# Performance work log

Hardware: AMD Instinct MI355X
Metric: run time of the kernel (lower is better)

Reference implementation:

```python
import jax, jax.numpy as jnp
import numpy as np

N = 100000
E = 1600000
D_PCA = 50
D_BIO = 64
HID = 32
HEADS = 4
OUT = 50
EPS = 1e-5


def setup_inputs() -> dict:
    key = jax.random.key(0)
    ks = jax.random.split(key, 32)
    g = lambda i, shape, s=0.05: jax.random.normal(ks[i], shape, dtype=jnp.float32) * s
    inp = {
        'x_pca': jax.random.normal(ks[0], (N, D_PCA), dtype=jnp.float32),
        'x_bio': jax.random.normal(ks[1], (N, D_BIO), dtype=jnp.float32),
        'edge_index': jax.random.randint(ks[2], (2, E), 0, N, dtype=jnp.int32),
        # bio encoder: Linear(64,16) -> BN(16) -> ELU -> Linear(16,16) -> ELU
        'bioW1': g(3, (16, D_BIO)), 'biob1': g(4, (16,)),
        'bn0_g': 1.0 + g(5, (16,)), 'bn0_b': g(6, (16,)),
        'bn0_m': g(7, (16,)), 'bn0_v': 1.0 + 0.1 * jax.random.uniform(ks[8], (16,), dtype=jnp.float32),
        'bioW2': g(9, (16, 16)), 'biob2': g(10, (16,)),
        # GATv2 layer 1: in = 50+16 = 66, out = HEADS*HID concat
        'Wl1': g(11, (HEADS * HID, D_PCA + 16)), 'bl1': g(12, (HEADS * HID,)),
        'Wr1': g(13, (HEADS * HID, D_PCA + 16)), 'br1': g(14, (HEADS * HID,)),
        'att1': g(15, (HEADS, HID)), 'bias1': g(16, (HEADS * HID,)),
        'bn1_g': 1.0 + g(17, (HEADS * HID,)), 'bn1_b': g(18, (HEADS * HID,)),
        'bn1_m': g(19, (HEADS * HID,)), 'bn1_v': 1.0 + 0.1 * jax.random.uniform(ks[20], (HEADS * HID,), dtype=jnp.float32),
        # GATv2 layer 2: in = HEADS*HID, heads=1, concat=False
        'Wl2': g(21, (HID, HEADS * HID)), 'bl2': g(22, (HID,)),
        'Wr2': g(23, (HID, HEADS * HID)), 'br2': g(24, (HID,)),
        'att2': g(25, (1, HID)), 'bias2': g(26, (HID,)),
        'bn2_g': 1.0 + g(27, (HID,)), 'bn2_b': g(28, (HID,)),
        'bn2_m': g(29, (HID,)), 'bn2_v': 1.0 + 0.1 * jax.random.uniform(ks[30], (HID,), dtype=jnp.float32),
        'predW': g(31, (OUT, HID)), 'predb': jnp.zeros((OUT,), dtype=jnp.float32),
    }
    return inp


def _bn(h, gm, bt, mean, var):
    # BatchNorm1d in eval mode (running stats)
    return (h - mean) * jax.lax.rsqrt(var + EPS) * gm + bt


def _gatv2(x, src, dst, Wl, bl, Wr, br, att, bias, heads, out_dim, concat):
    n = x.shape[0]
    xl = (x @ Wl.T + bl).reshape(n, heads, out_dim)  # source transform
    xr = (x @ Wr.T + br).reshape(n, heads, out_dim)  # target transform
    e = jax.nn.leaky_relu(xl[src] + xr[dst], 0.2)    # [E,H,C]
    logits = jnp.einsum('ehc,hc->eh', e, att)        # [E,H]
    m = jax.ops.segment_max(logits, dst, num_segments=n)
    a = jnp.exp(logits - m[dst])
    denom = jax.ops.segment_sum(a, dst, num_segments=n)
    alpha = a / (denom[dst] + 1e-16)                 # segment softmax over dst
    out = jax.ops.segment_sum(xl[src] * alpha[..., None], dst, num_segments=n)
    out = out.reshape(n, heads * out_dim) if concat else out.mean(axis=1)
    return out + bias


def reference(x_pca, x_bio, edge_index,
              bioW1, biob1, bn0_g, bn0_b, bn0_m, bn0_v, bioW2, biob2,
              Wl1, bl1, Wr1, br1, att1, bias1, bn1_g, bn1_b, bn1_m, bn1_v,
              Wl2, bl2, Wr2, br2, att2, bias2, bn2_g, bn2_b, bn2_m, bn2_v,
              predW, predb):
    n = x_pca.shape[0]
    # add self-loops (PyG GATv2Conv default)
    loop = jnp.arange(n, dtype=edge_index.dtype)
    src = jnp.concatenate([edge_index[0], loop])
    dst = jnp.concatenate([edge_index[1], loop])

    # bio encoder
    h_bio = jax.nn.elu(_bn(x_bio @ bioW1.T + biob1, bn0_g, bn0_b, bn0_m, bn0_v))
    h_bio = jax.nn.elu(h_bio @ bioW2.T + biob2)
    x = jnp.concatenate([x_pca, h_bio], axis=1)  # [N, 66]

    h = _gatv2(x, src, dst, Wl1, bl1, Wr1, br1, att1, bias1, HEADS, HID, True)
    h = jax.nn.elu(_bn(h, bn1_g, bn1_b, bn1_m, bn1_v))  # dropout off (eval)
    h = _gatv2(h, src, dst, Wl2, bl2, Wr2, br2, att2, bias2, 1, HID, False)
    h = jax.nn.elu(_bn(h, bn2_g, bn2_b, bn2_m, bn2_v))
    return h @ predW.T + predb
```

## Files before the change

kernel.cpp:

```cpp
#include <hip/hip_runtime.h>
#include <hip/hip_fp16.h>
#include <cstdint>
#include <cstddef>

#define NN 100000
#define NE 1600000
#define NEP (NE + NN)
#define NBLK 200
#define CHUNK ((NEP + NBLK - 1) / NBLK)
#define NBUCK2 ((NN + 255) / 256)
#define HISTN (NBUCK2 * NBLK)
#define HSCAN_BLOCKS ((HISTN + 1023) / 1024)

typedef __attribute__((ext_vector_type(8))) _Float16 half8;
typedef __attribute__((ext_vector_type(4))) _Float16 h4v;
typedef __attribute__((ext_vector_type(2))) _Float16 h2v;
typedef __attribute__((ext_vector_type(4))) float float4v;

__device__ __forceinline__ float elu_f(float x) {
    return x > 0.f ? x : __expf(x) - 1.f;
}

template<int CTRL>
__device__ __forceinline__ float dpp_add(float x) {
    int s = __builtin_amdgcn_update_dpp(0, __float_as_int(x), CTRL, 0xF, 0xF, true);
    return x + __int_as_float(s);
}
__device__ __forceinline__ float sum8_all(float x) {
    x = dpp_add<0xB1>(x); x = dpp_add<0x4E>(x); x = dpp_add<0x141>(x);
    return x;
}
__device__ __forceinline__ float sum16_all(float x) {
    x = dpp_add<0xB1>(x); x = dpp_add<0x4E>(x); x = dpp_add<0x141>(x); x = dpp_add<0x140>(x);
    return x;
}

__device__ __forceinline__ float dot2f(h2v a, h2v b, float c) {
#if __has_builtin(__builtin_amdgcn_fdot2)
    return __builtin_amdgcn_fdot2(a, b, c, false);
#else
    return fmaf((float)a[0], (float)b[0], fmaf((float)a[1], (float)b[1], c));
#endif
}

__device__ __forceinline__ h2v hmax2v(h2v a, h2v b) {
#if __has_builtin(__builtin_elementwise_max)
    return __builtin_elementwise_max(a, b);
#else
    __half2 r = __hmax2(*(__half2*)&a, *(__half2*)&b);
    return *(h2v*)&r;
#endif
}


__global__ __launch_bounds__(256) void part_hist(const int* __restrict__ ei, int* __restrict__ hist)
{
    __shared__ int cnt[NBUCK2];
    int tid = threadIdx.x, k = blockIdx.x;
    for (int i = tid; i < NBUCK2; i += 256) cnt[i] = 0;
    __syncthreads();
    int e0 = k * CHUNK, e1 = min(e0 + CHUNK, NEP);
    for (int e = e0 + tid; e < e1; e += 256) {
        int dst = (e < NE) ? ei[NE + e] : e - NE;
        atomicAdd(&cnt[dst >> 8], 1);
    }
    __syncthreads();
    for (int i = tid; i < NBUCK2; i += 256) hist[i * NBLK + k] = cnt[i];
}

__global__ __launch_bounds__(256) void scan_p1(const int* __restrict__ src, int* __restrict__ part, int n)
{
    __shared__ int wsum[4];
    int t = threadIdx.x;
    int i0 = blockIdx.x * 1024 + t * 4;
    int s = 0;
    if (i0 + 3 < n) { int4 d = *(const int4*)(src + i0); s = d.x + d.y + d.z + d.w; }
    else { for (int k = 0; k < 4; k++) if (i0 + k < n) s += src[i0 + k]; }
    for (int d = 1; d < 64; d <<= 1) s += __shfl_xor(s, d, 64);
    if ((t & 63) == 0) wsum[t >> 6] = s;
    __syncthreads();
    if (t == 0) part[blockIdx.x] = wsum[0] + wsum[1] + wsum[2] + wsum[3];
}

__global__ __launch_bounds__(128) void scan_p2(int* __restrict__ part, int nb, int* __restrict__ off)
{
    __shared__ int wt[2];
    int t = threadIdx.x;
    int lane = t & 63, w = t >> 6;
    int v = (t < nb) ? part[t] : 0;
    int x = v;
    for (int d = 1; d < 64; d <<= 1) { int y = __shfl_up(x, d, 64); if (lane >= d) x += y; }
    if (lane == 63) wt[w] = x;
    __syncthreads();
    int base = (w == 1) ? wt[0] : 0;
    int excl = base + x - v;
    if (t < nb) part[t] = excl;
    if (t == 0) off[NN] = NEP;
}

__global__ __launch_bounds__(256) void scan_p3(int* __restrict__ data, const int* __restrict__ part, int n)
{
    __shared__ int wsum[4];
    int t = threadIdx.x, lane = t & 63, w = t >> 6;
    int i0 = blockIdx.x * 1024 + t * 4;
    int d0 = 0, d1 = 0, d2 = 0, d3 = 0;
    if (i0 + 3 < n) { int4 d = *(const int4*)(data + i0); d0 = d.x; d1 = d.y; d2 = d.z; d3 = d.w; }
    else if (i0 < n) {
        d0 = data[i0];
        if (i0 + 1 < n) d1 = data[i0 + 1];
        if (i0 + 2 < n) d2 = data[i0 + 2];
    }
    int s = d0 + d1 + d2 + d3;
    int x = s;
    for (int d = 1; d < 64; d <<= 1) { int y = __shfl_up(x, d, 64); if (lane >= d) x += y; }
    if (lane == 63) wsum[w] = x;
    __syncthreads();
    int wb = 0;
    for (int i = 0; i < w; i++) wb += wsum[i];
    int base = part[blockIdx.x] + wb + x - s;
    if (i0 < n)     data[i0]     = base;
    if (i0 + 1 < n) data[i0 + 1] = base + d0;
    if (i0 + 2 < n) data[i0 + 2] = base + d0 + d1;
    if (i0 + 3 < n) data[i0 + 3] = base + d0 + d1 + d2;
}

__global__ __launch_bounds__(256) void part_scatter(const int* __restrict__ ei,
                                                    const int* __restrict__ hist,
                                                    unsigned* __restrict__ ebuf)
{
    __shared__ int cur[NBUCK2];
    int tid = threadIdx.x, k = blockIdx.x;
    for (int i = tid; i < NBUCK2; i += 256) cur[i] = hist[i * NBLK + k];
    __syncthreads();
    int e0 = k * CHUNK, e1 = min(e0 + CHUNK, NEP);
    for (int e = e0 + tid; e < e1; e += 256) {
        int src, dst;
        if (e < NE) { src = ei[e]; dst = ei[NE + e]; } else { src = dst = e - NE; }
        int pos = atomicAdd(&cur[dst >> 8], 1);
        ebuf[pos] = (unsigned)src | ((unsigned)(dst & 255) << 24);
    }
}

__global__ __launch_bounds__(256) void bucket_csr(const int* __restrict__ hist,
                                                  const unsigned* __restrict__ ebuf,
                                                  int* __restrict__ off, int* __restrict__ csr)
{
    __shared__ int cnt[256];
    __shared__ int cur[256];
    __shared__ int wsum[4];
    int b = blockIdx.x;
    int d0 = b << 8;
    int tid = threadIdx.x;
    int e0 = hist[b * NBLK];
    int e1 = (b + 1 < NBUCK2) ? hist[(b + 1) * NBLK] : NEP;
    cnt[tid] = 0;
    __syncthreads();
    for (int i = e0 + tid; i < e1; i += 256) atomicAdd(&cnt[ebuf[i] >> 24], 1);
    __syncthreads();
    int c = cnt[tid];
    int x = c;
    int lane = tid & 63, w = tid >> 6;
    for (int d = 1; d < 64; d <<= 1) { int y = __shfl_up(x, d, 64); if (lane >= d) x += y; }
    if (lane == 63) wsum[w] = x;
    __syncthreads();
    int wb = 0;
    for (int i = 0; i < w; i++) wb += wsum[i];
    int excl = wb + x - c;
    cur[tid] = e0 + excl;
    int node = d0 + tid;
    if (node < NN) off[node] = e0 + excl;
    __syncthreads();
    for (int i = e0 + tid; i < e1; i += 256) {
        unsigned v = ebuf[i];
        int p = atomicAdd(&cur[v >> 24], 1);
        csr[p] = (int)(v & 0xFFFFFF);
    }
}


__global__ __launch_bounds__(256) void bio_kernel(
    const float* __restrict__ xb, const float* __restrict__ xp,
    const float* __restrict__ W1, const float* __restrict__ b1,
    const float* __restrict__ g0, const float* __restrict__ bb0,
    const float* __restrict__ m0, const float* __restrict__ v0,
    const float* __restrict__ W2, const float* __restrict__ b2,
    __half* __restrict__ xh)
{
    __shared__ float sW1[16*64], sW2[16*16], sb1[16], sb2[16], ss[16], st[16];
    int tid = threadIdx.x;
    for (int idx = tid; idx < 1024; idx += 256) sW1[idx] = W1[idx];
    if (tid < 256) sW2[tid] = W2[tid];
    if (tid < 16) {
        sb1[tid] = b1[tid]; sb2[tid] = b2[tid];
        float s = g0[tid] * rsqrtf(v0[tid] + 1e-5f);
        ss[tid] = s; st[tid] = bb0[tid] - m0[tid] * s;
    }
    __syncthreads();
    int i = blockIdx.x * 256 + tid;
    if (i >= NN) return;
    float bio[64];
    const float4* p = (const float4*)(xb + (size_t)i * 64);
    #pragma unroll
    for (int q = 0; q < 16; q++) {
        float4 f = p[q];
        bio[q*4] = f.x; bio[q*4+1] = f.y; bio[q*4+2] = f.z; bio[q*4+3] = f.w;
    }
    float t1[16];
    #pragma unroll
    for (int j = 0; j < 16; j++) {
        float acc = sb1[j];
        #pragma unroll
        for (int k = 0; k < 64; k++) acc += bio[k] * sW1[j*64 + k];
        acc = acc * ss[j] + st[j];
        t1[j] = elu_f(acc);
    }
    __half* xrow = xh + (size_t)i * 96;
    const float* xpr = xp + (size_t)i * 50;
    #pragma unroll
    for (int j = 0; j < 25; j++) {
        float2 f = *(const float2*)(xpr + 2 * j);
        *(__half2*)(xrow + 2 * j) = __floats2half2_rn(f.x, f.y);
    }
    #pragma unroll
    for (int j = 0; j < 16; j++) {
        float acc = sb2[j];
        #pragma unroll
        for (int k = 0; k < 16; k++) acc += t1[k] * sW2[j*16 + k];
        xrow[50 + j] = __float2half(elu_f(acc));
    }
    __half2 z2 = __floats2half2_rn(0.f, 0.f);
    #pragma unroll
    for (int j = 0; j < 15; j++) *(__half2*)(xrow + 66 + 2 * j) = z2;
}


__global__ __launch_bounds__(256) void wconvert_all(
    const float* __restrict__ Wl1, const float* __restrict__ Wr1,
    const float* __restrict__ bl1, const float* __restrict__ br1,
    const float* __restrict__ Wl2, const float* __restrict__ Wr2,
    const float* __restrict__ bl2, const float* __restrict__ br2,
    const float* __restrict__ predW, const float* __restrict__ predb,
    __half* __restrict__ wcat1, float* __restrict__ bcat1,
    __half* __restrict__ wcat2, float* __restrict__ bcat2,
    __half* __restrict__ wpred, float* __restrict__ bpred)
{
    int t = blockIdx.x * 256 + threadIdx.x;
    if (t < 256 * 96) {
        int j = t / 96, k = t - j * 96;
        float v = (k < 66) ? ((j < 128) ? Wl1[j * 66 + k] : Wr1[(j - 128) * 66 + k]) : 0.f;
        wcat1[t] = __float2half(v);
    }
    int u = t - 256 * 96;
    if (u >= 0 && u < 64 * 128) {
        int j = u >> 7, k = u & 127;
        float v = (j < 32) ? Wl2[j * 128 + k] : Wr2[(j - 32) * 128 + k];
        wcat2[u] = __float2half(v);
    }
    int w = u - 64 * 128;
    if (w >= 0 && w < 64 * 32) {
        int j = w >> 5;
        wpred[w] = __float2half(j < 50 ? predW[w] : 0.f);
    }
    int z = w - 64 * 32;
    if (z >= 0 && z < 256) bcat1[z] = (z < 128) ? bl1[z] : br1[z - 128];
    int z2 = z - 256;
    if (z2 >= 0 && z2 < 64) bcat2[z2] = (z2 < 32) ? bl2[z2] : br2[z2 - 32];
    int z3 = z2 - 64;
    if (z3 >= 0 && z3 < 64) bpred[z3] = (z3 < 50) ? predb[z3] : 0.f;
}

template<int KT, int NC, bool FOUT>
__global__ __launch_bounds__(256) void mfma_gemm(
    const __half* __restrict__ in, const __half* __restrict__ wcat,
    const float* __restrict__ bcat, void* __restrict__ outv, int n, int ncol)
{
    constexpr int K = KT * 32;
    constexpr int KP = K + 8;
    __shared__ __half sW[NC * KP];
    __shared__ __half sX[64 * KP];
    __shared__ float sB[NC];
    int tid = threadIdx.x;
    for (int idx = tid * 8; idx < NC * K; idx += 256 * 8) {
        int r = idx / K, c = idx - r * K;
        *(half8*)(&sW[r * KP + c]) = *(const half8*)(&wcat[r * K + c]);
    }
    for (int idx = tid; idx < NC; idx += 256) sB[idx] = bcat[idx];
    int row0 = blockIdx.x * 64;
    half8 hz = {0, 0, 0, 0, 0, 0, 0, 0};
    for (int idx = tid * 8; idx < 64 * K; idx += 256 * 8) {
        int r = idx / K, c = idx - r * K;
        int gr = row0 + r;
        half8 v = (gr < n) ? *(const half8*)(&in[(size_t)gr * K + c]) : hz;
        *(half8*)(&sX[r * KP + c]) = v;
    }
    __syncthreads();
    int w = tid >> 6, lane = tid & 63;
    int m = lane & 15, quad = lane >> 4;
    half8 a[KT];
    #pragma unroll
    for (int kt = 0; kt < KT; kt++)
        a[kt] = *(const half8*)(&sX[(w * 16 + m) * KP + kt * 32 + quad * 8]);
    #pragma unroll 1
    for (int nt = 0; nt < NC / 16; nt++) {
        float4v acc = {0.f, 0.f, 0.f, 0.f};
        #pragma unroll
        for (int kt = 0; kt < KT; kt++) {
            half8 bfrag = *(const half8*)(&sW[(nt * 16 + m) * KP + kt * 32 + quad * 8]);
            acc = __builtin_amdgcn_mfma_f32_16x16x32_f16(a[kt], bfrag, acc, 0, 0, 0);
        }
        int col = nt * 16 + m;
        float bias = sB[col];
        #pragma unroll
        for (int i = 0; i < 4; i++) {
            int r = row0 + w * 16 + quad * 4 + i;
            if (r < n) {
                if (FOUT) { if (col < ncol) ((float*)outv)[(size_t)r * ncol + col] = acc[i] + bias; }
                else ((__half*)outv)[(size_t)r * NC + col] = __float2half(acc[i] + bias);
            }
        }
    }
}

__global__ __launch_bounds__(256) void fused_gat1(
    const int* __restrict__ off, const int* __restrict__ csr,
    const __half* __restrict__ xcat, const float* __restrict__ att,
    const float* __restrict__ bias, const float* __restrict__ g,
    const float* __restrict__ b, const float* __restrict__ m,
    const float* __restrict__ v, __half* __restrict__ h1)
{
    int wave = threadIdx.x >> 6;
    int lane = threadIdx.x & 63;
    int node = blockIdx.x * 4 + wave;
    if (node >= NN) return;
    int slot = lane >> 5;
    int l = lane & 31;
    int ch = l * 4;

    h4v xr4 = *(const h4v*)(xcat + (size_t)node * 256 + 128 + ch);
    h2v xr01 = {xr4[0], xr4[1]}, xr23 = {xr4[2], xr4[3]};
    float4 af = *(const float4*)(att + ch);
    h2v a01 = {(_Float16)af.x, (_Float16)af.y};
    h2v a23 = {(_Float16)af.z, (_Float16)af.w};
    const h2v c2 = {(_Float16)0.2f, (_Float16)0.2f};

    int k0 = off[node], k1 = off[node + 1];
    float acc0 = 0.f, acc1 = 0.f, acc2 = 0.f, acc3 = 0.f, denom = 0.f;

    for (int base = k0; base < k1; base += 64) {
        int nb = min(64, k1 - base);
        int mysrc = (lane < nb) ? csr[base + lane] : 0;
        int p0 = __builtin_amdgcn_readlane(mysrc, 0);
        int p1 = __builtin_amdgcn_readlane(mysrc, nb > 1 ? 1 : 0);
        int ssel = slot ? p1 : p0;
        h4v cur = *(const h4v*)(xcat + (size_t)(unsigned)ssel * 256 + ch);
        for (int t = 0; t < nb; t += 2) {
            int t2 = (t + 2 < nb) ? t + 2 : nb - 1;
            int t3 = (t + 3 < nb) ? t + 3 : nb - 1;
            int n0 = __builtin_amdgcn_readlane(mysrc, t2);
            int n1 = __builtin_amdgcn_readlane(mysrc, t3);
            int nsel = slot ? n1 : n0;
            h4v nxt = *(const h4v*)(xcat + (size_t)(unsigned)nsel * 256 + ch);

            h2v xl01 = {cur[0], cur[1]}, xl23 = {cur[2], cur[3]};
            h2v s01 = xl01 + xr01, s23 = xl23 + xr23;
            h2v ls01 = hmax2v(s01, s01 * c2);
            h2v ls23 = hmax2v(s23, s23 * c2);
            float pp = dot2f(ls01, a01, dot2f(ls23, a23, 0.f));
            pp = sum8_all(pp);
            bool valid = (t + slot) < nb;
            float wgt = valid ? __expf(pp) : 0.f;
            denom += wgt;
            acc0 = fmaf((float)cur[0], wgt, acc0);
            acc1 = fmaf((float)cur[1], wgt, acc1);
            acc2 = fmaf((float)cur[2], wgt, acc2);
            acc3 = fmaf((float)cur[3], wgt, acc3);
            cur = nxt;
        }
    }
    acc0 += __shfl_xor(acc0, 32, 64);
    acc1 += __shfl_xor(acc1, 32, 64);
    acc2 += __shfl_xor(acc2, 32, 64);
    acc3 += __shfl_xor(acc3, 32, 64);
    denom += __shfl_xor(denom, 32, 64);
    if (slot == 0) {
        float inv = 1.f / (denom + 1e-16f);
        float4 gv = *(const float4*)(g + ch);
        float4 vv = *(const float4*)(v + ch);
        float4 bv = *(const float4*)(b + ch);
        float4 mv = *(const float4*)(m + ch);
        float4 biv = *(const float4*)(bias + ch);
        float s0 = gv.x * rsqrtf(vv.x + 1e-5f);
        float s1 = gv.y * rsqrtf(vv.y + 1e-5f);
        float s2 = gv.z * rsqrtf(vv.z + 1e-5f);
        float s3 = gv.w * rsqrtf(vv.w + 1e-5f);
        float o0 = elu_f((acc0 * inv + biv.x) * s0 + (bv.x - mv.x * s0));
        float o1 = elu_f((acc1 * inv + biv.y) * s1 + (bv.y - mv.y * s1));
        float o2 = elu_f((acc2 * inv + biv.z) * s2 + (bv.z - mv.z * s2));
        float o3 = elu_f((acc3 * inv + biv.w) * s3 + (bv.w - mv.w * s3));
        h4v o = {(_Float16)o0, (_Float16)o1, (_Float16)o2, (_Float16)o3};
        *(h4v*)(h1 + (size_t)node * 128 + ch) = o;
    }
}

__global__ __launch_bounds__(256) void fused_gat2(
    const int* __restrict__ off, const int* __restrict__ csr,
    const __half* __restrict__ xcat2, const float* __restrict__ att,
    const float* __restrict__ bias, const float* __restrict__ g,
    const float* __restrict__ b, const float* __restrict__ m,
    const float* __restrict__ v, __half* __restrict__ h2)
{
    int wave = threadIdx.x >> 6;
    int lane = threadIdx.x & 63;
    int node = blockIdx.x * 4 + wave;
    if (node >= NN) return;
    int row = lane >> 4;
    int cp  = lane & 15;
    int c   = cp * 2;

    h2v xr = *(const h2v*)(xcat2 + (size_t)node * 64 + 32 + c);
    float2 af = *(const float2*)(att + c);
    h2v ah = {(_Float16)af.x, (_Float16)af.y};
    const h2v c2 = {(_Float16)0.2f, (_Float16)0.2f};

    int k0 = off[node], k1 = off[node + 1];
    float accx = 0.f, accy = 0.f, denom = 0.f;

    for (int base = k0; base < k1; base += 64) {
        int nb = min(64, k1 - base);
        int mysrc = (lane < nb) ? csr[base + lane] : 0;
        for (int t = 0; t < nb; t += 4) {
            int i1 = min(t + 1, nb - 1), i2 = min(t + 2, nb - 1), i3 = min(t + 3, nb - 1);
            int s0 = __builtin_amdgcn_readlane(mysrc, t);
            int s1 = __builtin_amdgcn_readlane(mysrc, i1);
            int s2 = __builtin_amdgcn_readlane(mysrc, i2);
            int s3 = __builtin_amdgcn_readlane(mysrc, i3);
            int sa  = (row & 1) ? s1 : s0;
            int sb_ = (row & 1) ? s3 : s2;
            int ss  = (row & 2) ? sb_ : sa;
            h2v xl = *(const h2v*)(xcat2 + (size_t)(unsigned)ss * 64 + c);
            h2v s = xl + xr;
            h2v ls = hmax2v(s, s * c2);
            float pp = dot2f(ls, ah, 0.f);
            pp = sum16_all(pp);
            bool valid = (t + row) < nb;
            float wgt = valid ? __expf(pp) : 0.f;
            denom += wgt;
            accx = fmaf((float)xl[0], wgt, accx);
            accy = fmaf((float)xl[1], wgt, accy);
        }
    }
    accx  += __shfl_xor(accx, 16, 64);  accx  += __shfl_xor(accx, 32, 64);
    accy  += __shfl_xor(accy, 16, 64);  accy  += __shfl_xor(accy, 32, 64);
    denom += __shfl_xor(denom, 16, 64); denom += __shfl_xor(denom, 32, 64);
    if (row == 0) {
        float inv = 1.f / (denom + 1e-16f);
        float sC0 = g[c]     * rsqrtf(v[c]     + 1e-5f);
        float sC1 = g[c + 1] * rsqrtf(v[c + 1] + 1e-5f);
        float o0 = elu_f((accx * inv + bias[c])     * sC0 + (b[c]     - m[c]     * sC0));
        float o1 = elu_f((accy * inv + bias[c + 1]) * sC1 + (b[c + 1] - m[c + 1] * sC1));
        *(__half2*)(h2 + (size_t)node * 32 + c) = __floats2half2_rn(o0, o1);
    }
}

extern "C" void kernel_launch(void* const* d_in, const int* in_sizes, int n_in,
                              void* d_out, int out_size, void* d_ws, size_t ws_size,
                              hipStream_t stream)
{
    const float* x_pca = (const float*)d_in[0];
    const float* x_bio = (const float*)d_in[1];
    const int*   ei    = (const int*)d_in[2];
    const float* bioW1 = (const float*)d_in[3];
    const float* biob1 = (const float*)d_in[4];
    const float* bn0_g = (const float*)d_in[5];
    const float* bn0_b = (const float*)d_in[6];
    const float* bn0_m = (const float*)d_in[7];
    const float* bn0_v = (const float*)d_in[8];
    const float* bioW2 = (const float*)d_in[9];
    const float* biob2 = (const float*)d_in[10];
    const float* Wl1   = (const float*)d_in[11];
    const float* bl1   = (const float*)d_in[12];
    const float* Wr1   = (const float*)d_in[13];
    const float* br1   = (const float*)d_in[14];
    const float* att1  = (const float*)d_in[15];
    const float* bias1 = (const float*)d_in[16];
    const float* bn1_g = (const float*)d_in[17];
    const float* bn1_b = (const float*)d_in[18];
    const float* bn1_m = (const float*)d_in[19];
    const float* bn1_v = (const float*)d_in[20];
    const float* Wl2   = (const float*)d_in[21];
    const float* bl2   = (const float*)d_in[22];
    const float* Wr2   = (const float*)d_in[23];
    const float* br2   = (const float*)d_in[24];
    const float* att2  = (const float*)d_in[25];
    const float* bias2 = (const float*)d_in[26];
    const float* bn2_g = (const float*)d_in[27];
    const float* bn2_b = (const float*)d_in[28];
    const float* bn2_m = (const float*)d_in[29];
    const float* bn2_v = (const float*)d_in[30];
    const float* predW = (const float*)d_in[31];
    const float* predb = (const float*)d_in[32];

    float* ws = (float*)d_ws;
    __half* xh    = (__half*)ws;
    float*  p0    = ws + 4800000;
    __half* xcat1 = (__half*)p0;
    float*  p1    = p0 + 12800000;
    __half* h1h   = (__half*)p1;
    float*  p2    = p1 + 6400000;
    __half* xcat2 = (__half*)p2;
    float*  p3    = p2 + 3200000;
    __half* h2h   = (__half*)p3;
    float*  p4    = p3 + 1600000;
    __half* wcat1 = (__half*)p4;
    float*  bcat1 = p4 + 12288;
    __half* wcat2 = (__half*)(bcat1 + 256);
    float*  bcat2 = bcat1 + 256 + 4096;
    __half* wpred = (__half*)(bcat2 + 64);
    float*  bpred = bcat2 + 64 + 1024;
    int*    ib    = (int*)(bpred + 64);
    unsigned* ebuf = (unsigned*)ib;
    int*    hist   = ib + NEP;
    int*    part   = hist + HISTN;
    int*    off    = part + 128;
    int*    csr    = off + NN + 1;

    float* out = (float*)d_out;

    part_hist<<<NBLK, 256, 0, stream>>>(ei, hist);
    scan_p1<<<HSCAN_BLOCKS, 256, 0, stream>>>(hist, part, HISTN);
    scan_p2<<<1, 128, 0, stream>>>(part, HSCAN_BLOCKS, off);
    scan_p3<<<HSCAN_BLOCKS, 256, 0, stream>>>(hist, part, HISTN);
    part_scatter<<<NBLK, 256, 0, stream>>>(ei, hist, ebuf);
    bucket_csr<<<NBUCK2, 256, 0, stream>>>(hist, ebuf, off, csr);

    bio_kernel<<<(NN + 255) / 256, 256, 0, stream>>>(
        x_bio, x_pca, bioW1, biob1, bn0_g, bn0_b, bn0_m, bn0_v, bioW2, biob2, xh);

    wconvert_all<<<138, 256, 0, stream>>>(
        Wl1, Wr1, bl1, br1, Wl2, Wr2, bl2, br2, predW, predb,
        wcat1, bcat1, wcat2, bcat2, wpred, bpred);

    mfma_gemm<3, 256, false><<<(NN + 63) / 64, 256, 0, stream>>>(xh, wcat1, bcat1, xcat1, NN, 0);

    fused_gat1<<<(NN + 3) / 4, 256, 0, stream>>>(
        off, csr, xcat1, att1, bias1, bn1_g, bn1_b, bn1_m, bn1_v, h1h);

    mfma_gemm<4, 64, false><<<(NN + 63) / 64, 256, 0, stream>>>(h1h, wcat2, bcat2, xcat2, NN, 0);

    fused_gat2<<<(NN + 3) / 4, 256, 0, stream>>>(
        off, csr, xcat2, att2, bias2, bn2_g, bn2_b, bn2_m, bn2_v, h2h);

    mfma_gemm<1, 64, true><<<(NN + 63) / 64, 256, 0, stream>>>(h2h, wpred, bpred, out, NN, 50);
}
```

Measured before the change: 432.3 us.

## Widen per-lane gathers in GAT kernels and make GEMMs persistent with direct A loads

```diff
diff --git a/kernel.cpp b/kernel.cpp
--- a/kernel.cpp
+++ b/kernel.cpp
@@ -4,6 +4,7 @@
 #include <cstddef>
 
 #define NN 100000
+#define NROWS 100032
 #define NE 1600000
 #define NEP (NE + NN)
 #define NBLK 200
@@ -11,9 +12,9 @@
 #define NBUCK2 ((NN + 255) / 256)
 #define HISTN (NBUCK2 * NBLK)
 #define HSCAN_BLOCKS ((HISTN + 1023) / 1024)
+#define NT64 ((NN + 63) / 64)
 
 typedef __attribute__((ext_vector_type(8))) _Float16 half8;
-typedef __attribute__((ext_vector_type(4))) _Float16 h4v;
 typedef __attribute__((ext_vector_type(2))) _Float16 h2v;
 typedef __attribute__((ext_vector_type(4))) float float4v;
 
@@ -26,12 +27,9 @@
     int s = __builtin_amdgcn_update_dpp(0, __float_as_int(x), CTRL, 0xF, 0xF, true);
     return x + __int_as_float(s);
 }
-__device__ __forceinline__ float sum8_all(float x) {
-    x = dpp_add<0xB1>(x); x = dpp_add<0x4E>(x); x = dpp_add<0x141>(x);
-    return x;
-}
-__device__ __forceinline__ float sum16_all(float x) {
-    x = dpp_add<0xB1>(x); x = dpp_add<0x4E>(x); x = dpp_add<0x141>(x); x = dpp_add<0x140>(x);
+__device__ __forceinline__ float sum2_all(float x) { return dpp_add<0xB1>(x); }
+__device__ __forceinline__ float sum4_all(float x) {
+    x = dpp_add<0xB1>(x); x = dpp_add<0x4E>(x);
     return x;
 }
 
@@ -272,12 +270,11 @@
 template<int KT, int NC, bool FOUT>
 __global__ __launch_bounds__(256) void mfma_gemm(
     const __half* __restrict__ in, const __half* __restrict__ wcat,
-    const float* __restrict__ bcat, void* __restrict__ outv, int n, int ncol)
+    const float* __restrict__ bcat, void* __restrict__ outv, int n, int ncol, int ntiles)
 {
     constexpr int K = KT * 32;
     constexpr int KP = K + 8;
     __shared__ __half sW[NC * KP];
-    __shared__ __half sX[64 * KP];
     __shared__ float sB[NC];
     int tid = threadIdx.x;
     for (int idx = tid * 8; idx < NC * K; idx += 256 * 8) {
@@ -285,37 +282,32 @@
         *(half8*)(&sW[r * KP + c]) = *(const half8*)(&wcat[r * K + c]);
     }
     for (int idx = tid; idx < NC; idx += 256) sB[idx] = bcat[idx];
-    int row0 = blockIdx.x * 64;
-    half8 hz = {0, 0, 0, 0, 0, 0, 0, 0};
-    for (int idx = tid * 8; idx < 64 * K; idx += 256 * 8) {
-        int r = idx / K, c = idx - r * K;
-        int gr = row0 + r;
-        half8 v = (gr < n) ? *(const half8*)(&in[(size_t)gr * K + c]) : hz;
-        *(half8*)(&sX[r * KP + c]) = v;
-    }
     __syncthreads();
     int w = tid >> 6, lane = tid & 63;
     int m = lane & 15, quad = lane >> 4;
-    half8 a[KT];
-    #pragma unroll
-    for (int kt = 0; kt < KT; kt++)
-        a[kt] = *(const half8*)(&sX[(w * 16 + m) * KP + kt * 32 + quad * 8]);
-    #pragma unroll 1
-    for (int nt = 0; nt < NC / 16; nt++) {
-        float4v acc = {0.f, 0.f, 0.f, 0.f};
+    for (int tile = blockIdx.x; tile < ntiles; tile += gridDim.x) {
+        int arow = tile * 64 + w * 16 + m;
+        const __half* inr = in + (size_t)arow * K + quad * 8;
+        half8 a[KT];
         #pragma unroll
-        for (int kt = 0; kt < KT; kt++) {
-            half8 bfrag = *(const half8*)(&sW[(nt * 16 + m) * KP + kt * 32 + quad * 8]);
-            acc = __builtin_amdgcn_mfma_f32_16x16x32_f16(a[kt], bfrag, acc, 0, 0, 0);
-        }
-        int col = nt * 16 + m;
-        float bias = sB[col];
-        #pragma unroll
-        for (int i = 0; i < 4; i++) {
-            int r = row0 + w * 16 + quad * 4 + i;
-            if (r < n) {
-                if (FOUT) { if (col < ncol) ((float*)outv)[(size_t)r * ncol + col] = acc[i] + bias; }
-                else ((__half*)outv)[(size_t)r * NC + col] = __float2half(acc[i] + bias);
+        for (int kt = 0; kt < KT; kt++) a[kt] = *(const half8*)(inr + kt * 32);
+        #pragma unroll 1
+        for (int nt = 0; nt < NC / 16; nt++) {
+            float4v acc = {0.f, 0.f, 0.f, 0.f};
+            #pragma unroll
+            for (int kt = 0; kt < KT; kt++) {
+                half8 bfrag = *(const half8*)(&sW[(nt * 16 + m) * KP + kt * 32 + quad * 8]);
+                acc = __builtin_amdgcn_mfma_f32_16x16x32_f16(a[kt], bfrag, acc, 0, 0, 0);
+            }
+            int col = nt * 16 + m;
+            float bias = sB[col];
+            #pragma unroll
+            for (int i = 0; i < 4; i++) {
+                int r = tile * 64 + w * 16 + quad * 4 + i;
+                if (r < n) {
+                    if (FOUT) { if (col < ncol) ((float*)outv)[(size_t)r * ncol + col] = acc[i] + bias; }
+                    else ((__half*)outv)[(size_t)r * NC + col] = __float2half(acc[i] + bias);
+                }
             }
         }
     }
@@ -332,73 +324,98 @@
     int lane = threadIdx.x & 63;
     int node = blockIdx.x * 4 + wave;
     if (node >= NN) return;
-    int slot = lane >> 5;
-    int l = lane & 31;
-    int ch = l * 4;
-
-    h4v xr4 = *(const h4v*)(xcat + (size_t)node * 256 + 128 + ch);
-    h2v xr01 = {xr4[0], xr4[1]}, xr23 = {xr4[2], xr4[3]};
-    float4 af = *(const float4*)(att + ch);
-    h2v a01 = {(_Float16)af.x, (_Float16)af.y};
-    h2v a23 = {(_Float16)af.z, (_Float16)af.w};
+    int row = lane >> 3;
+    int cl  = lane & 7;
+    int ch  = cl * 16;
+
+    half8 xrA = *(const half8*)(xcat + (size_t)node * 256 + 128 + ch);
+    half8 xrB = *(const half8*)(xcat + (size_t)node * 256 + 128 + ch + 8);
+    h2v ath[8];
+    #pragma unroll
+    for (int q = 0; q < 4; q++) {
+        float4 af = *(const float4*)(att + ch + 4 * q);
+        ath[2*q]   = h2v{(_Float16)af.x, (_Float16)af.y};
+        ath[2*q+1] = h2v{(_Float16)af.z, (_Float16)af.w};
+    }
     const h2v c2 = {(_Float16)0.2f, (_Float16)0.2f};
 
     int k0 = off[node], k1 = off[node + 1];
-    float acc0 = 0.f, acc1 = 0.f, acc2 = 0.f, acc3 = 0.f, denom = 0.f;
+    float acc[16];
+    #pragma unroll
+    for (int i = 0; i < 16; i++) acc[i] = 0.f;
+    float denom = 0.f;
 
     for (int base = k0; base < k1; base += 64) {
         int nb = min(64, k1 - base);
         int mysrc = (lane < nb) ? csr[base + lane] : 0;
-        int p0 = __builtin_amdgcn_readlane(mysrc, 0);
-        int p1 = __builtin_amdgcn_readlane(mysrc, nb > 1 ? 1 : 0);
-        int ssel = slot ? p1 : p0;
-        h4v cur = *(const h4v*)(xcat + (size_t)(unsigned)ssel * 256 + ch);
-        for (int t = 0; t < nb; t += 2) {
-            int t2 = (t + 2 < nb) ? t + 2 : nb - 1;
-            int t3 = (t + 3 < nb) ? t + 3 : nb - 1;
-            int n0 = __builtin_amdgcn_readlane(mysrc, t2);
-            int n1 = __builtin_amdgcn_readlane(mysrc, t3);
-            int nsel = slot ? n1 : n0;
-            h4v nxt = *(const h4v*)(xcat + (size_t)(unsigned)nsel * 256 + ch);
-
-            h2v xl01 = {cur[0], cur[1]}, xl23 = {cur[2], cur[3]};
-            h2v s01 = xl01 + xr01, s23 = xl23 + xr23;
-            h2v ls01 = hmax2v(s01, s01 * c2);
-            h2v ls23 = hmax2v(s23, s23 * c2);
-            float pp = dot2f(ls01, a01, dot2f(ls23, a23, 0.f));
-            pp = sum8_all(pp);
-            bool valid = (t + slot) < nb;
+        int nbm1 = nb - 1;
+        int ss = __shfl(mysrc, min(row, nbm1), 64);
+        const __half* xrow0 = xcat + (size_t)(unsigned)ss * 256 + ch;
+        half8 curA = *(const half8*)xrow0;
+        half8 curB = *(const half8*)(xrow0 + 8);
+        for (int t = 0; t < nb; t += 8) {
+            int ns = __shfl(mysrc, min(t + 8 + row, nbm1), 64);
+            const __half* xrown = xcat + (size_t)(unsigned)ns * 256 + ch;
+            half8 nxtA = *(const half8*)xrown;
+            half8 nxtB = *(const half8*)(xrown + 8);
+
+            float pp = 0.f;
+            #pragma unroll
+            for (int i = 0; i < 4; i++) {
+                h2v xl = {curA[2*i], curA[2*i+1]};
+                h2v xr = {xrA[2*i], xrA[2*i+1]};
+                h2v s = xl + xr;
+                h2v l = hmax2v(s, s * c2);
+                pp = dot2f(l, ath[i], pp);
+            }
+            #pragma unroll
+            for (int i = 0; i < 4; i++) {
+                h2v xl = {curB[2*i], curB[2*i+1]};
+                h2v xr = {xrB[2*i], xrB[2*i+1]};
+                h2v s = xl + xr;
+                h2v l = hmax2v(s, s * c2);
+                pp = dot2f(l, ath[4+i], pp);
+            }
+            pp = sum2_all(pp);
+            bool valid = (t + row) < nb;
             float wgt = valid ? __expf(pp) : 0.f;
             denom += wgt;
-            acc0 = fmaf((float)cur[0], wgt, acc0);
-            acc1 = fmaf((float)cur[1], wgt, acc1);
-            acc2 = fmaf((float)cur[2], wgt, acc2);
-            acc3 = fmaf((float)cur[3], wgt, acc3);
-            cur = nxt;
+            #pragma unroll
+            for (int i = 0; i < 8; i++) acc[i] = fmaf((float)curA[i], wgt, acc[i]);
+            #pragma unroll
+            for (int i = 0; i < 8; i++) acc[8+i] = fmaf((float)curB[i], wgt, acc[8+i]);
+            curA = nxtA; curB = nxtB;
         }
     }
-    acc0 += __shfl_xor(acc0, 32, 64);
-    acc1 += __shfl_xor(acc1, 32, 64);
-    acc2 += __shfl_xor(acc2, 32, 64);
-    acc3 += __shfl_xor(acc3, 32, 64);
+    #pragma unroll
+    for (int i = 0; i < 16; i++) {
+        acc[i] += __shfl_xor(acc[i], 8, 64);
+        acc[i] += __shfl_xor(acc[i], 16, 64);
+        acc[i] += __shfl_xor(acc[i], 32, 64);
+    }
+    denom += __shfl_xor(denom, 8, 64);
+    denom += __shfl_xor(denom, 16, 64);
     denom += __shfl_xor(denom, 32, 64);
-    if (slot == 0) {
+    if (row == 0) {
         float inv = 1.f / (denom + 1e-16f);
-        float4 gv = *(const float4*)(g + ch);
-        float4 vv = *(const float4*)(v + ch);
-        float4 bv = *(const float4*)(b + ch);
-        float4 mv = *(const float4*)(m + ch);
-        float4 biv = *(const float4*)(bias + ch);
-        float s0 = gv.x * rsqrtf(vv.x + 1e-5f);
-        float s1 = gv.y * rsqrtf(vv.y + 1e-5f);
-        float s2 = gv.z * rsqrtf(vv.z + 1e-5f);
-        float s3 = gv.w * rsqrtf(vv.w + 1e-5f);
-        float o0 = elu_f((acc0 * inv + biv.x) * s0 + (bv.x - mv.x * s0));
-        float o1 = elu_f((acc1 * inv + biv.y) * s1 + (bv.y - mv.y * s1));
-        float o2 = elu_f((acc2 * inv + biv.z) * s2 + (bv.z - mv.z * s2));
-        float o3 = elu_f((acc3 * inv + biv.w) * s3 + (bv.w - mv.w * s3));
-        h4v o = {(_Float16)o0, (_Float16)o1, (_Float16)o2, (_Float16)o3};
-        *(h4v*)(h1 + (size_t)node * 128 + ch) = o;
+        _Float16 oh[16];
+        #pragma unroll
+        for (int q = 0; q < 4; q++) {
+            float4 gv = *(const float4*)(g + ch + 4*q);
+            float4 vv = *(const float4*)(v + ch + 4*q);
+            float4 bv = *(const float4*)(b + ch + 4*q);
+            float4 mv = *(const float4*)(m + ch + 4*q);
+            float4 iv = *(const float4*)(bias + ch + 4*q);
+            float sc;
+            sc = gv.x * rsqrtf(vv.x + 1e-5f); oh[4*q+0] = (_Float16)elu_f((acc[4*q+0] * inv + iv.x) * sc + (bv.x - mv.x * sc));
+            sc = gv.y * rsqrtf(vv.y + 1e-5f); oh[4*q+1] = (_Float16)elu_f((acc[4*q+1] * inv + iv.y) * sc + (bv.y - mv.y * sc));
+            sc = gv.z * rsqrtf(vv.z + 1e-5f); oh[4*q+2] = (_Float16)elu_f((acc[4*q+2] * inv + iv.z) * sc + (bv.z - mv.z * sc));
+            sc = gv.w * rsqrtf(vv.w + 1e-5f); oh[4*q+3] = (_Float16)elu_f((acc[4*q+3] * inv + iv.w) * sc + (bv.w - mv.w * sc));
+        }
+        half8 oA = {oh[0], oh[1], oh[2], oh[3], oh[4], oh[5], oh[6], oh[7]};
+        half8 oB = {oh[8], oh[9], oh[10], oh[11], oh[12], oh[13], oh[14], oh[15]};
+        *(half8*)(h1 + (size_t)node * 128 + ch) = oA;
+        *(half8*)(h1 + (size_t)node * 128 + ch + 8) = oB;
     }
 }
 
@@ -413,52 +430,83 @@
     int lane = threadIdx.x & 63;
     int node = blockIdx.x * 4 + wave;
     if (node >= NN) return;
-    int row = lane >> 4;
-    int cp  = lane & 15;
-    int c   = cp * 2;
-
-    h2v xr = *(const h2v*)(xcat2 + (size_t)node * 64 + 32 + c);
-    float2 af = *(const float2*)(att + c);
-    h2v ah = {(_Float16)af.x, (_Float16)af.y};
+    int row = lane >> 2;
+    int cl  = lane & 3;
+    int ch  = cl * 8;
+
+    half8 xr8 = *(const half8*)(xcat2 + (size_t)node * 64 + 32 + ch);
+    h2v ath[4];
+    #pragma unroll
+    for (int q = 0; q < 2; q++) {
+        float4 af = *(const float4*)(att + ch + 4 * q);
+        ath[2*q]   = h2v{(_Float16)af.x, (_Float16)af.y};
+        ath[2*q+1] = h2v{(_Float16)af.z, (_Float16)af.w};
+    }
     const h2v c2 = {(_Float16)0.2f, (_Float16)0.2f};
 
     int k0 = off[node], k1 = off[node + 1];
-    float accx = 0.f, accy = 0.f, denom = 0.f;
+    float acc[8];
+    #pragma unroll
+    for (int i = 0; i < 8; i++) acc[i] = 0.f;
+    float denom = 0.f;
 
     for (int base = k0; base < k1; base += 64) {
         int nb = min(64, k1 - base);
         int mysrc = (lane < nb) ? csr[base + lane] : 0;
-        for (int t = 0; t < nb; t += 4) {
-            int i1 = min(t + 1, nb - 1), i2 = min(t + 2, nb - 1), i3 = min(t + 3, nb - 1);
-            int s0 = __builtin_amdgcn_readlane(mysrc, t);
-            int s1 = __builtin_amdgcn_readlane(mysrc, i1);
-            int s2 = __builtin_amdgcn_readlane(mysrc, i2);
-            int s3 = __builtin_amdgcn_readlane(mysrc, i3);
-            int sa  = (row & 1) ? s1 : s0;
-            int sb_ = (row & 1) ? s3 : s2;
-            int ss  = (row & 2) ? sb_ : sa;
-            h2v xl = *(const h2v*)(xcat2 + (size_t)(unsigned)ss * 64 + c);
-            h2v s = xl + xr;
-            h2v ls = hmax2v(s, s * c2);
-            float pp = dot2f(ls, ah, 0.f);
-            pp = sum16_all(pp);
+        int nbm1 = nb - 1;
+        int ss = __shfl(mysrc, min(row, nbm1), 64);
+        half8 cur = *(const half8*)(xcat2 + (size_t)(unsigned)ss * 64 + ch);
+        for (int t = 0; t < nb; t += 16) {
+            int ns = __shfl(mysrc, min(t + 16 + row, nbm1), 64);
+            half8 nxt = *(const half8*)(xcat2 + (size_t)(unsigned)ns * 64 + ch);
+
+            float pp = 0.f;
+            #pragma unroll
+            for (int i = 0; i < 4; i++) {
+                h2v xl = {cur[2*i], cur[2*i+1]};
+                h2v xr = {xr8[2*i], xr8[2*i+1]};
+                h2v s = xl + xr;
+                h2v l = hmax2v(s, s * c2);
+                pp = dot2f(l, ath[i], pp);
+            }
+            pp = sum4_all(pp);
             bool valid = (t + row) < nb;
             float wgt = valid ? __expf(pp) : 0.f;
             denom += wgt;
-            accx = fmaf((float)xl[0], wgt, accx);
-            accy = fmaf((float)xl[1], wgt, accy);
+            #pragma unroll
+            for (int i = 0; i < 8; i++) acc[i] = fmaf((float)cur[i], wgt, acc[i]);
+            cur = nxt;
         }
     }
-    accx  += __shfl_xor(accx, 16, 64);  accx  += __shfl_xor(accx, 32, 64);
-    accy  += __shfl_xor(accy, 16, 64);  accy  += __shfl_xor(accy, 32, 64);
-    denom += __shfl_xor(denom, 16, 64); denom += __shfl_xor(denom, 32, 64);
+    #pragma unroll
+    for (int i = 0; i < 8; i++) {
+        acc[i] += __shfl_xor(acc[i], 4, 64);
+        acc[i] += __shfl_xor(acc[i], 8, 64);
+        acc[i] += __shfl_xor(acc[i], 16, 64);
+        acc[i] += __shfl_xor(acc[i], 32, 64);
+    }
+    denom += __shfl_xor(denom, 4, 64);
+    denom += __shfl_xor(denom, 8, 64);
+    denom += __shfl_xor(denom, 16, 64);
+    denom += __shfl_xor(denom, 32, 64);
     if (row == 0) {
         float inv = 1.f / (denom + 1e-16f);
-        float sC0 = g[c]     * rsqrtf(v[c]     + 1e-5f);
-        float sC1 = g[c + 1] * rsqrtf(v[c + 1] + 1e-5f);
-        float o0 = elu_f((accx * inv + bias[c])     * sC0 + (b[c]     - m[c]     * sC0));
-        float o1 = elu_f((accy * inv + bias[c + 1]) * sC1 + (b[c + 1] - m[c + 1] * sC1));
-        *(__half2*)(h2 + (size_t)node * 32 + c) = __floats2half2_rn(o0, o1);
+        _Float16 oh[8];
+        #pragma unroll
+        for (int q = 0; q < 2; q++) {
+            float4 gv = *(const float4*)(g + ch + 4*q);
+            float4 vv = *(const float4*)(v + ch + 4*q);
+            float4 bv = *(const float4*)(b + ch + 4*q);
+            float4 mv = *(const float4*)(m + ch + 4*q);
+            float4 iv = *(const float4*)(bias + ch + 4*q);
+            float sc;
+            sc = gv.x * rsqrtf(vv.x + 1e-5f); oh[4*q+0] = (_Float16)elu_f((acc[4*q+0] * inv + iv.x) * sc + (bv.x - mv.x * sc));
+            sc = gv.y * rsqrtf(vv.y + 1e-5f); oh[4*q+1] = (_Float16)elu_f((acc[4*q+1] * inv + iv.y) * sc + (bv.y - mv.y * sc));
+            sc = gv.z * rsqrtf(vv.z + 1e-5f); oh[4*q+2] = (_Float16)elu_f((acc[4*q+2] * inv + iv.z) * sc + (bv.z - mv.z * sc));
+            sc = gv.w * rsqrtf(vv.w + 1e-5f); oh[4*q+3] = (_Float16)elu_f((acc[4*q+3] * inv + iv.w) * sc + (bv.w - mv.w * sc));
+        }
+        half8 o = {oh[0], oh[1], oh[2], oh[3], oh[4], oh[5], oh[6], oh[7]};
+        *(half8*)(h2 + (size_t)node * 32 + ch) = o;
     }
 }
 
@@ -502,15 +550,15 @@
 
     float* ws = (float*)d_ws;
     __half* xh    = (__half*)ws;
-    float*  p0    = ws + 4800000;
+    float*  p0    = ws + 4801536;
     __half* xcat1 = (__half*)p0;
-    float*  p1    = p0 + 12800000;
+    float*  p1    = p0 + 12804096;
     __half* h1h   = (__half*)p1;
-    float*  p2    = p1 + 6400000;
+    float*  p2    = p1 + 6402048;
     __half* xcat2 = (__half*)p2;
-    float*  p3    = p2 + 3200000;
+    float*  p3    = p2 + 3201024;
     __half* h2h   = (__half*)p3;
-    float*  p4    = p3 + 1600000;
+    float*  p4    = p3 + 1600512;
     __half* wcat1 = (__half*)p4;
     float*  bcat1 = p4 + 12288;
     __half* wcat2 = (__half*)(bcat1 + 256);
@@ -540,15 +588,15 @@
         Wl1, Wr1, bl1, br1, Wl2, Wr2, bl2, br2, predW, predb,
         wcat1, bcat1, wcat2, bcat2, wpred, bpred);
 
-    mfma_gemm<3, 256, false><<<(NN + 63) / 64, 256, 0, stream>>>(xh, wcat1, bcat1, xcat1, NN, 0);
+    mfma_gemm<3, 256, false><<<768, 256, 0, stream>>>(xh, wcat1, bcat1, xcat1, NN, 0, NT64);
 
     fused_gat1<<<(NN + 3) / 4, 256, 0, stream>>>(
         off, csr, xcat1, att1, bias1, bn1_g, bn1_b, bn1_m, bn1_v, h1h);
 
-    mfma_gemm<4, 64, false><<<(NN + 63) / 64, 256, 0, stream>>>(h1h, wcat2, bcat2, xcat2, NN, 0);
+    mfma_gemm<4, 64, false><<<768, 256, 0, stream>>>(h1h, wcat2, bcat2, xcat2, NN, 0, NT64);
 
     fused_gat2<<<(NN + 3) / 4, 256, 0, stream>>>(
         off, csr, xcat2, att2, bias2, bn2_g, bn2_b, bn2_m, bn2_v, h2h);
 
-    mfma_gemm<1, 64, true><<<(NN + 63) / 64, 256, 0, stream>>>(h2h, wpred, bpred, out, NN, 50);
-}
+    mfma_gemm<1, 64, true><<<768, 256, 0, stream>>>(h2h, wpred, bpred, out, NN, 50, NT64);
+}
```

Result: slower. 461.9 us (+6.9%).
